# Optimization experiments

Hardware: AMD Instinct MI355X
Metric: run time of the kernel (lower is better)

Reference implementation:

```python
import jax, jax.numpy as jnp
import numpy as np

B, L, H = 8, 1024, 512
CHUNK = 16  # query-row chunk size for the score computation; L % CHUNK == 0


def setup_inputs() -> dict:
    key = jax.random.key(0)
    ks = jax.random.split(key, 6)
    s = 1.0 / np.sqrt(H)  # torch nn.Linear default init bound
    return {
        "inputs": jax.random.normal(ks[0], (B, L, H), jnp.float32),
        "W1": jax.random.uniform(ks[1], (H, H), jnp.float32, -s, s),
        "b1": jax.random.uniform(ks[2], (H,), jnp.float32, -s, s),
        "W2": jax.random.uniform(ks[3], (H, H), jnp.float32, -s, s),
        "b2": jax.random.uniform(ks[4], (H,), jnp.float32, -s, s),
        # torch: nn.init.normal_(q, mean=-0.02, std=0.02)
        "q": jax.random.normal(ks[5], (H,), jnp.float32) * 0.02 - 0.02,
    }


def _scores(u1, u2, q):
    # u[b,i,j] = tanh(u1[b,i,:] + u2[b,j,:]) . q  -- computed in row-chunks to
    # avoid materializing the full [B,L,L,H] tensor the torch loop implies.
    Bx, Lx, Hx = u1.shape
    n = Lx // CHUNK
    u1c = u1.reshape(Bx, n, CHUNK, Hx).transpose(1, 0, 2, 3)  # [n, B, c, H]

    def step(carry, u1_i):
        t = jnp.tanh(u1_i[:, :, None, :] + u2[:, None, :, :])  # [B, c, L, H]
        return carry, jnp.einsum('bclh,h->bcl', t, q)

    _, s = jax.lax.scan(jax.checkpoint(step), None, u1c)  # [n, B, c, L]
    return s.transpose(1, 0, 2, 3).reshape(Bx, Lx, Lx)


def reference(inputs, W1, b1, W2, b2, q):
    u1 = inputs @ W1.T + b1  # [B, L, H]
    u2 = inputs @ W2.T + b2  # [B, L, H]
    u = _scores(u1, u2, q)   # [B, L, L]
    # relu=False in init, so no relu on u
    a = jax.nn.softmax(u, axis=2)
    h = jnp.einsum('bij,bjh->bih', a, inputs)  # [B, L, H]
    return h, a
```

## Files before the change

kernel.cpp:

```cpp
#include <hip/hip_runtime.h>

typedef _Float16 f16;
typedef _Float16 f16x2 __attribute__((ext_vector_type(2)));
typedef _Float16 f16x4 __attribute__((ext_vector_type(4)));
typedef _Float16 f16x8 __attribute__((ext_vector_type(8)));
typedef float f32x4 __attribute__((ext_vector_type(4)));

#define LOG2E_X2 2.8853900817779268f

__constant__ float D8[8] = {0.543915f, 0.177997f, 0.0652351f, 0.0242575f,
                            0.00903807f, 0.00336823f, 0.00125536f, 0.000467884f};

static __device__ __forceinline__ void gl2lds16(const void* g, void* l) {
  __builtin_amdgcn_global_load_lds((const __attribute__((address_space(1))) void*)g,
                                   (__attribute__((address_space(3))) void*)l, 16, 0, 0);
}


__global__ __launch_bounds__(256) void k_prep_x(const float* __restrict__ X,
                                                f16* __restrict__ Xh, f16* __restrict__ XhT) {
  const int ht = blockIdx.x, it = blockIdx.y, b = blockIdx.z;
  __shared__ f16 Lt[64][72];
  const int t = threadIdx.x;
  const int r = t >> 4, c4 = (t & 15) * 4;
  const float* Xb = X + ((size_t)b * 1024 + it * 64) * 512 + ht * 64;
#pragma unroll
  for (int k = 0; k < 4; ++k) {
    const int rr = r + 16 * k;
    float4 v = *(const float4*)&Xb[(size_t)rr * 512 + c4];
    f16 h0 = (f16)v.x, h1 = (f16)v.y, h2 = (f16)v.z, h3 = (f16)v.w;
    *(f16x4*)&Xh[((size_t)b * 1024 + it * 64 + rr) * 512 + ht * 64 + c4] = {h0, h1, h2, h3};
    Lt[c4 + 0][rr] = h0; Lt[c4 + 1][rr] = h1; Lt[c4 + 2][rr] = h2; Lt[c4 + 3][rr] = h3;
  }
  __syncthreads();
  const int hr = t >> 2, seg = t & 3;
  f16* dst = &XhT[((size_t)b * 512 + ht * 64 + hr) * 1024 + it * 64 + seg * 16];
  *(f16x8*)(dst) = *(const f16x8*)&Lt[hr][seg * 16];
  *(f16x8*)(dst + 8) = *(const f16x8*)&Lt[hr][seg * 16 + 8];
}

__global__ __launch_bounds__(256) void k_prep_w(const float* __restrict__ W1,
                                                const float* __restrict__ W2,
                                                f16* __restrict__ Wh) {
  const int row = blockIdx.x, z = blockIdx.y, t = threadIdx.x;
  const float* W = z ? W2 : W1;
  float2 v = *(const float2*)&W[(size_t)row * 512 + t * 2];
  *(f16x2*)&Wh[(size_t)z * 262144 + (size_t)row * 512 + t * 2] = {(f16)v.x, (f16)v.y};
}

__global__ void k_prep_b(const float* __restrict__ b1, const float* __restrict__ b2,
                         float* __restrict__ biasCat) {
  const int t = blockIdx.x * 256 + threadIdx.x;
  biasCat[t] = t < 512 ? b1[t] : b2[t - 512];
}

template <int NM>
__global__ __launch_bounds__(256) void k_trig(const float* __restrict__ u,
                                              const float* __restrict__ q,
                                              f16* __restrict__ At, f16* __restrict__ Bt,
                                              float* __restrict__ qa, float* __restrict__ qb,
                                              int m0, int wq) {
  const int i = blockIdx.x, t = threadIdx.x;
  const float w = 0.62831853f;
  const float2 a2 = *(const float2*)&u[(size_t)i * 1024 + 2 * t];
  const float2 b2 = *(const float2*)&u[(size_t)i * 1024 + 512 + 2 * t];
  const float2 q2 = *(const float2*)&q[2 * t];
  if (wq) {
    float sa = q2.x * a2.x + q2.y * a2.y;
    float sb = q2.x * b2.x + q2.y * b2.y;
#pragma unroll
    for (int o = 1; o < 64; o <<= 1) { sa += __shfl_xor(sa, o); sb += __shfl_xor(sb, o); }
    __shared__ float red[8];
    const int lane = t & 63, widx = t >> 6;
    if (lane == 0) { red[widx] = sa; red[4 + widx] = sb; }
    __syncthreads();
    if (t == 0) qa[i] = red[0] + red[1] + red[2] + red[3];
    if (t == 1) qb[i] = red[4] + red[5] + red[6] + red[7];
  }
  float s1[4], c1[4], sm_[4], cm_[4];
  const float ang[4] = {w * a2.x, w * a2.y, w * b2.x, w * b2.y};
#pragma unroll
  for (int uu = 0; uu < 4; ++uu) {
    __sincosf(ang[uu], &s1[uu], &c1[uu]);
    if (m0 == 1) { sm_[uu] = s1[uu]; cm_[uu] = c1[uu]; }
    else __sincosf(m0 * ang[uu], &sm_[uu], &cm_[uu]);
  }
  const size_t ldT = (size_t)NM * 1024;
  f16* Ar = At + (size_t)i * ldT + 2 * t;
  f16* Br = Bt + (size_t)i * ldT + 2 * t;
#pragma unroll
  for (int j = 0; j < NM; ++j) {
    const float dm = D8[m0 - 1 + j];
    const float qdx = q2.x * dm, qdy = q2.y * dm;
    *(f16x2*)(Ar + j * 1024)       = {(f16)(qdx * sm_[0]), (f16)(qdy * sm_[1])};
    *(f16x2*)(Ar + j * 1024 + 512) = {(f16)(qdx * cm_[0]), (f16)(qdy * cm_[1])};
    *(f16x2*)(Br + j * 1024)       = {(f16)cm_[2], (f16)cm_[3]};
    *(f16x2*)(Br + j * 1024 + 512) = {(f16)sm_[2], (f16)sm_[3]};
    if (j + 1 < NM) {
#pragma unroll
      for (int uu = 0; uu < 4; ++uu) {
        const float ns = sm_[uu] * c1[uu] + cm_[uu] * s1[uu];
        const float nc = cm_[uu] * c1[uu] - sm_[uu] * s1[uu];
        sm_[uu] = ns; cm_[uu] = nc;
      }
    }
  }
}

template <int MODE, int ACC, int T, int WR, int WC, int FI, int FJ>
__global__ __launch_bounds__(T, 2) void k_gemmG(
    const f16* __restrict__ A, const f16* __restrict__ B, float* __restrict__ C,
    const float* __restrict__ bias0, int Kloop, int ldAB, long halfA, long halfC) {
  constexpr int BM = WR * FI * 16;
  constexpr int BN = WC * FJ * 16;
  __shared__ alignas(16) char smA[2][BM * 128];
  __shared__ alignas(16) char smB[2][BN * 128];
  const int t = threadIdx.x;
  int nx, my, z;
  if (MODE == 1) {
    const int lin = blockIdx.x;
    const int xcd = lin & 7, s = lin >> 3;
    const int g = xcd + 8 * (s >> 2);
    nx = s & 3; my = g & 3; z = g >> 2;
  } else {
    nx = blockIdx.x; my = blockIdx.y; z = blockIdx.z;
  }
  const f16* Ab; const f16* Bb; float* Cb; const float* bias = nullptr;
  int ldC;
  if (MODE == 0) {
    Ab = A + (size_t)my * BM * ldAB;
    Bb = B + (size_t)nx * BN * ldAB;
    Cb = C + (size_t)my * BM * 1024 + nx * BN;
    bias = bias0 + nx * BN;
    ldC = 1024;
  } else if (MODE == 1) {
    const int b = z & 7, h = z >> 3;
    Ab = A + ((size_t)(b * 1024 + my * 256)) * ldAB + h * halfA;
    Bb = B + ((size_t)(b * 1024 + nx * 256)) * ldAB + h * halfA;
    Cb = C + h * halfC + ((size_t)(b * 1024 + my * 256)) * 1024 + nx * 256;
    ldC = 1024;
  } else {
    Ab = A + (size_t)z * 1048576 + (size_t)my * BM * ldAB;
    Bb = B + (size_t)z * 524288 + (size_t)nx * BN * ldAB;
    Cb = C + (size_t)z * 524288 + (size_t)my * BM * 512 + nx * BN;
    ldC = 512;
  }
  const int wid = t >> 6, lane = t & 63;
  const int wr = wid / WC, wc = wid % WC;
  const int rl = lane & 15, kc = lane >> 4;
  f32x4 acc[FI][FJ] = {};

  auto stage = [&](int buf, int kt) {
    const f16* gA = Ab + kt * 64;
    const f16* gB = Bb + kt * 64;
    constexpr int LA = BM * 8 / T, LB = BN * 8 / T;
#pragma unroll
    for (int ii = 0; ii < LA; ++ii) {
      const int idx = ii * T + t;
      const int row = idx >> 3, c = idx & 7;
      gl2lds16(gA + (size_t)row * ldAB + ((c ^ (row & 7)) * 8),
               smA[buf] + ii * (T * 16) + wid * 1024);
    }
#pragma unroll
    for (int ii = 0; ii < LB; ++ii) {
      const int idx = ii * T + t;
      const int row = idx >> 3, c = idx & 7;
      gl2lds16(gB + (size_t)row * ldAB + ((c ^ (row & 7)) * 8),
               smB[buf] + ii * (T * 16) + wid * 1024);
    }
  };

  const int nkt = Kloop >> 6;
  stage(0, 0);
  __syncthreads();
  for (int kt = 0; kt < nkt; ++kt) {
    const int cur = kt & 1;
    if (kt + 1 < nkt) stage(cur ^ 1, kt + 1);
    const char* lA = smA[cur];
    const char* lB = smB[cur];
#pragma unroll
    for (int kk = 0; kk < 2; ++kk) {
      f16x8 av[FI], bv[FJ];
#pragma unroll
      for (int fi = 0; fi < FI; ++fi) {
        const int rloc = (wr * FI + fi) * 16 + rl;
        av[fi] = *(const f16x8*)(lA + rloc * 128 + (((kc + 4 * kk) ^ (rloc & 7)) << 4));
      }
#pragma unroll
      for (int fj = 0; fj < FJ; ++fj) {
        const int cloc = (wc * FJ + fj) * 16 + rl;
        bv[fj] = *(const f16x8*)(lB + cloc * 128 + (((kc + 4 * kk) ^ (cloc & 7)) << 4));
      }
#pragma unroll
      for (int fi = 0; fi < FI; ++fi)
#pragma unroll
        for (int fj = 0; fj < FJ; ++fj)
          acc[fi][fj] = __builtin_amdgcn_mfma_f32_16x16x32_f16(av[fi], bv[fj], acc[fi][fj], 0, 0, 0);
    }
    __syncthreads();
  }

#pragma unroll
  for (int fj = 0; fj < FJ; ++fj) {
    const int gcol = (wc * FJ + fj) * 16 + rl;
    const float bvv = (MODE == 0) ? bias[gcol] : 0.f;
#pragma unroll
    for (int fi = 0; fi < FI; ++fi) {
      const int grow0 = (wr * FI + fi) * 16 + kc * 4;
      f32x4 v = acc[fi][fj];
#pragma unroll
      for (int r = 0; r < 4; ++r) {
        const size_t o = (size_t)(grow0 + r) * ldC + gcol;
        float x = v[r] + bvv;
        if (ACC) x += Cb[o];
        Cb[o] = x;
      }
    }
  }
}

__global__ __launch_bounds__(256) void k_softmax2(const float* __restrict__ P0,
                                                  const float* __restrict__ P1,
                                                  const float* __restrict__ qa,
                                                  const float* __restrict__ qb,
                                                  float* __restrict__ out_a,
                                                  f16* __restrict__ a16) {
  const int row = blockIdx.x, t = threadIdx.x;
  const int b = row >> 10;
  const size_t off = (size_t)row * 1024 + t * 4;
  float4 p0 = *(const float4*)(P0 + off);
  float4 p1 = *(const float4*)(P1 + off);
  float4 qb4 = *(const float4*)(qb + (size_t)b * 1024 + t * 4);
  const float qi = qa[row];
  float4 v;
  v.x = p0.x + p1.x + 0.2f * (qi + qb4.x);
  v.y = p0.y + p1.y + 0.2f * (qi + qb4.y);
  v.z = p0.z + p1.z + 0.2f * (qi + qb4.z);
  v.w = p0.w + p1.w + 0.2f * (qi + qb4.w);
  float m = fmaxf(fmaxf(v.x, v.y), fmaxf(v.z, v.w));
#pragma unroll
  for (int o = 1; o < 64; o <<= 1) m = fmaxf(m, __shfl_xor(m, o));
  __shared__ float red[4];
  const int w = t >> 6, ln = t & 63;
  if (ln == 0) red[w] = m;
  __syncthreads();
  m = fmaxf(fmaxf(red[0], red[1]), fmaxf(red[2], red[3]));
  v.x = __expf(v.x - m); v.y = __expf(v.y - m);
  v.z = __expf(v.z - m); v.w = __expf(v.w - m);
  float s = v.x + v.y + v.z + v.w;
#pragma unroll
  for (int o = 1; o < 64; o <<= 1) s += __shfl_xor(s, o);
  __syncthreads();
  if (ln == 0) red[w] = s;
  __syncthreads();
  s = red[0] + red[1] + red[2] + red[3];
  const float inv = 1.0f / s;
  v.x *= inv; v.y *= inv; v.z *= inv; v.w *= inv;
  *(float4*)(out_a + off) = v;
  *(f16x4*)(a16 + off) = {(f16)v.x, (f16)v.y, (f16)v.z, (f16)v.w};
}

typedef short s16x2 __attribute__((ext_vector_type(2)));

static __device__ __forceinline__ float fdot2f(f16x2 a, f16x2 b, float c) {
#if __has_builtin(__builtin_amdgcn_fdot2)
  return __builtin_amdgcn_fdot2(a, b, c, false);
#else
  return c + (float)a[0] * (float)b[0] + (float)a[1] * (float)b[1];
#endif
}

__global__ void k_qprep(const float* __restrict__ q, f16* __restrict__ qh,
                        float* __restrict__ qsum) {
  const int t = threadIdx.x;
  float v = q[t];
  qh[t] = (f16)v;
  float s = v;
#pragma unroll
  for (int o = 1; o < 64; o <<= 1) s += __shfl_xor(s, o);
  __shared__ float red[8];
  if ((t & 63) == 0) red[t >> 6] = s;
  __syncthreads();
  if (t == 0) {
    float tot = 0.f;
#pragma unroll
    for (int i = 0; i < 8; ++i) tot += red[i];
    *qsum = tot;
  }
}

__global__ __launch_bounds__(256) void k_gemm_exp(
    const float* __restrict__ X, const float* __restrict__ W1,
    const float* __restrict__ b1, const float* __restrict__ W2,
    const float* __restrict__ b2, f16* __restrict__ e1, f16* __restrict__ e2) {
  const int z = blockIdx.z;
  const float* W = z ? W2 : W1;
  const float* bias = z ? b2 : b1;
  f16* out = z ? e2 : e1;
  const int r0 = blockIdx.y * 64;
  const int c0 = blockIdx.x * 64;
  __shared__ alignas(16) float Xs[64][68];
  __shared__ alignas(16) float Ws[64][68];
  const int t = threadIdx.x;
  const int row = t >> 2, seg = t & 3;
  const int tr = t >> 4, tc = t & 15;
  float acc[4][4] = {};
#pragma unroll 1
  for (int k0 = 0; k0 < 512; k0 += 64) {
    const float4* gx = (const float4*)(X + (size_t)(r0 + row) * 512 + k0 + seg * 16);
    float4* lx = (float4*)(&Xs[row][seg * 16]);
    lx[0] = gx[0]; lx[1] = gx[1]; lx[2] = gx[2]; lx[3] = gx[3];
    const float4* gw = (const float4*)(W + (size_t)(c0 + row) * 512 + k0 + seg * 16);
    float4* lw = (float4*)(&Ws[row][seg * 16]);
    lw[0] = gw[0]; lw[1] = gw[1]; lw[2] = gw[2]; lw[3] = gw[3];
    __syncthreads();
#pragma unroll 4
    for (int kk = 0; kk < 64; kk += 4) {
      float4 av[4], bv[4];
#pragma unroll
      for (int ii = 0; ii < 4; ++ii) av[ii] = *(const float4*)&Xs[tr + 16 * ii][kk];
#pragma unroll
      for (int jj = 0; jj < 4; ++jj) bv[jj] = *(const float4*)&Ws[tc + 16 * jj][kk];
#pragma unroll
      for (int ii = 0; ii < 4; ++ii) {
#pragma unroll
        for (int jj = 0; jj < 4; ++jj) {
          acc[ii][jj] = fmaf(av[ii].x, bv[jj].x, acc[ii][jj]);
          acc[ii][jj] = fmaf(av[ii].y, bv[jj].y, acc[ii][jj]);
          acc[ii][jj] = fmaf(av[ii].z, bv[jj].z, acc[ii][jj]);
          acc[ii][jj] = fmaf(av[ii].w, bv[jj].w, acc[ii][jj]);
        }
      }
    }
    __syncthreads();
  }
#pragma unroll
  for (int ii = 0; ii < 4; ++ii) {
    const int r = r0 + tr + 16 * ii;
#pragma unroll
    for (int jj = 0; jj < 4; ++jj) {
      const int c = c0 + tc + 16 * jj;
      float u = acc[ii][jj] + bias[c];
      float val = u * LOG2E_X2 - 4.0f;
      val = fminf(6.6759f, fmaxf(-14.6759f, val));
      out[(size_t)r * 512 + c] = (f16)exp2f(val);
    }
  }
}

template <int P>
static __device__ __forceinline__ void tanh_dot_step(const f16x8 (&Av)[4],
                                                     const f16x8 (&Bv)[4],
                                                     const f16x8& Qv, float (&acc)[4][4],
                                                     int c256, int kmag, int two2) {
  f16x2 qp = __builtin_shufflevector(Qv, Qv, 2 * P, 2 * P + 1);
#pragma unroll
  for (int jj = 0; jj < 4; ++jj) {
    f16x2 bp = __builtin_shufflevector(Bv[jj], Bv[jj], 2 * P, 2 * P + 1);
#pragma unroll
    for (int ii = 0; ii < 4; ++ii) {
      f16x2 ap = __builtin_shufflevector(Av[ii], Av[ii], 2 * P, 2 * P + 1);
      f16x2 d, r, tt;
      asm("v_pk_fma_f16 %0, %3, %4, %5\n\t"
          "v_pk_sub_i16 %1, %6, %0\n\t"
          "v_pk_fma_f16 %2, %0, %1, %7 neg_lo:[1,0,0] neg_hi:[1,0,0]\n\t"
          "v_pk_mul_f16 %1, %1, %2\n\t"
          "v_pk_fma_f16 %2, %0, %1, %7 neg_lo:[1,0,0] neg_hi:[1,0,0]\n\t"
          "v_pk_mul_f16 %1, %1, %2"
          : "=&v"(d), "=&v"(r), "=&v"(tt)
          : "v"(ap), "v"(bp), "v"(c256), "v"(kmag), "v"(two2));
      acc[ii][jj] = fdot2f(r, qp, acc[ii][jj]);
    }
  }
}

__global__ __launch_bounds__(256) void k_scores(const f16* __restrict__ e1,
                                                const f16* __restrict__ e2,
                                                const f16* __restrict__ qh,
                                                const float* __restrict__ qsum_p,
                                                float* __restrict__ out_a) {
  const int b = blockIdx.z, it = blockIdx.y, jt = blockIdx.x;
  __shared__ alignas(16) f16 As[64][72];
  __shared__ alignas(16) f16 Bs[64][72];
  __shared__ alignas(16) f16 Qs[512];
  const int t = threadIdx.x;
  const size_t eA = (size_t)(b * 1024 + it * 64) * 512;
  const size_t eB = (size_t)(b * 1024 + jt * 64) * 512;
  if (t < 64) ((uint4*)Qs)[t] = ((const uint4*)qh)[t];
  const int row = t >> 2, seg = t & 3;
  const int tr = t >> 4, tc = t & 15;
  const int c256 = 0x1C001C00;
  const int kmag = 0x77987798;
  const int two2 = 0x40004000;
  float acc[4][4] = {};
#pragma unroll 1
  for (int h0 = 0; h0 < 512; h0 += 64) {
    const f16* gA = e1 + eA + (size_t)row * 512 + h0;
    const f16* gB = e2 + eB + (size_t)row * 512 + h0;
    *(uint4*)(&As[row][seg * 8]) = *(const uint4*)(gA + seg * 8);
    *(uint4*)(&As[row][seg * 8 + 32]) = *(const uint4*)(gA + seg * 8 + 32);
    *(uint4*)(&Bs[row][seg * 8]) = *(const uint4*)(gB + seg * 8);
    *(uint4*)(&Bs[row][seg * 8 + 32]) = *(const uint4*)(gB + seg * 8 + 32);
    __syncthreads();
#pragma unroll 2
    for (int g = 0; g < 8; ++g) {
      f16x8 Av[4], Bv[4], Qv;
#pragma unroll
      for (int ii = 0; ii < 4; ++ii) Av[ii] = *(const f16x8*)&As[tr + 16 * ii][g * 8];
#pragma unroll
      for (int jj = 0; jj < 4; ++jj) Bv[jj] = *(const f16x8*)&Bs[tc + 16 * jj][g * 8];
      Qv = *(const f16x8*)&Qs[h0 + g * 8];
      tanh_dot_step<0>(Av, Bv, Qv, acc, c256, kmag, two2);
      tanh_dot_step<1>(Av, Bv, Qv, acc, c256, kmag, two2);
      tanh_dot_step<2>(Av, Bv, Qv, acc, c256, kmag, two2);
      tanh_dot_step<3>(Av, Bv, Qv, acc, c256, kmag, two2);
    }
    __syncthreads();
  }
  const float qs = *qsum_p;
#pragma unroll
  for (int ii = 0; ii < 4; ++ii) {
    const size_t orow = (size_t)(b * 1024 + it * 64 + tr + 16 * ii) * 1024;
#pragma unroll
    for (int jj = 0; jj < 4; ++jj)
      out_a[orow + jt * 64 + tc + 16 * jj] = qs - acc[ii][jj] * (1.0f / 128.0f);
  }
}

__global__ __launch_bounds__(256) void k_softmax(float* __restrict__ a) {
  float* row = a + (size_t)blockIdx.x * 1024;
  const int t = threadIdx.x;
  float4 v = ((const float4*)row)[t];
  float m = fmaxf(fmaxf(v.x, v.y), fmaxf(v.z, v.w));
#pragma unroll
  for (int o = 1; o < 64; o <<= 1) m = fmaxf(m, __shfl_xor(m, o));
  __shared__ float red[4];
  const int w = t >> 6, ln = t & 63;
  if (ln == 0) red[w] = m;
  __syncthreads();
  m = fmaxf(fmaxf(red[0], red[1]), fmaxf(red[2], red[3]));
  v.x = __expf(v.x - m); v.y = __expf(v.y - m);
  v.z = __expf(v.z - m); v.w = __expf(v.w - m);
  float s = v.x + v.y + v.z + v.w;
#pragma unroll
  for (int o = 1; o < 64; o <<= 1) s += __shfl_xor(s, o);
  __syncthreads();
  if (ln == 0) red[w] = s;
  __syncthreads();
  s = red[0] + red[1] + red[2] + red[3];
  const float inv = 1.0f / s;
  v.x *= inv; v.y *= inv; v.z *= inv; v.w *= inv;
  ((float4*)row)[t] = v;
}

__global__ __launch_bounds__(256) void k_av(const float* __restrict__ a,
                                            const float* __restrict__ X,
                                            float* __restrict__ h) {
  const int b = blockIdx.z;
  const int i0 = blockIdx.y * 64;
  const int c0 = blockIdx.x * 64;
  __shared__ alignas(16) float As[64][68];
  __shared__ alignas(16) float Xs[64][68];
  const float* Ab = a + (size_t)b * 1024 * 1024;
  const float* Xb = X + (size_t)b * 1024 * 512;
  const int t = threadIdx.x;
  const int row = t >> 2, seg = t & 3;
  const int tr = t >> 4, tc = t & 15;
  float acc[4][4] = {};
#pragma unroll 1
  for (int k0 = 0; k0 < 1024; k0 += 64) {
    const float4* ga = (const float4*)(Ab + (size_t)(i0 + row) * 1024 + k0 + seg * 16);
    float4* la = (float4*)(&As[row][seg * 16]);
    la[0] = ga[0]; la[1] = ga[1]; la[2] = ga[2]; la[3] = ga[3];
    const float4* gx = (const float4*)(Xb + (size_t)(k0 + row) * 512 + c0 + seg * 16);
    float4* lx = (float4*)(&Xs[row][seg * 16]);
    lx[0] = gx[0]; lx[1] = gx[1]; lx[2] = gx[2]; lx[3] = gx[3];
    __syncthreads();
#pragma unroll 8
    for (int k = 0; k < 64; ++k) {
      float av[4], bv[4];
#pragma unroll
      for (int ii = 0; ii < 4; ++ii) av[ii] = As[tr + 16 * ii][k];
#pragma unroll
      for (int jj = 0; jj < 4; ++jj) bv[jj] = Xs[k][tc + 16 * jj];
#pragma unroll
      for (int ii = 0; ii < 4; ++ii) {
#pragma unroll
        for (int jj = 0; jj < 4; ++jj)
          acc[ii][jj] = fmaf(av[ii], bv[jj], acc[ii][jj]);
      }
    }
    __syncthreads();
  }
#pragma unroll
  for (int ii = 0; ii < 4; ++ii) {
    const size_t orow = (size_t)b * 1024 * 512 + (size_t)(i0 + tr + 16 * ii) * 512;
#pragma unroll
    for (int jj = 0; jj < 4; ++jj)
      h[orow + c0 + tc + 16 * jj] = acc[ii][jj];
  }
}

extern "C" void kernel_launch(void* const* d_in, const int* in_sizes, int n_in,
                              void* d_out, int out_size, void* d_ws, size_t ws_size,
                              hipStream_t stream) {
  const float* inputs = (const float*)d_in[0];
  const float* W1 = (const float*)d_in[1];
  const float* b1 = (const float*)d_in[2];
  const float* W2 = (const float*)d_in[3];
  const float* b2 = (const float*)d_in[4];
  const float* q = (const float*)d_in[5];

  float* out_h = (float*)d_out;
  float* out_a = out_h + 4194304;

  const size_t FIXED = 101781504ULL;
  const size_t PER_M = 33554432ULL;
  if (ws_size < FIXED + PER_M) {
    char* ws = (char*)d_ws;
    f16* e1 = (f16*)ws;
    f16* e2 = (f16*)(ws + 8388608);
    f16* qh = (f16*)(ws + 16777216);
    float* qsum = (float*)(ws + 16778240);
    k_qprep<<<1, 512, 0, stream>>>(q, qh, qsum);
    k_gemm_exp<<<dim3(8, 128, 2), 256, 0, stream>>>(inputs, W1, b1, W2, b2, e1, e2);
    k_scores<<<dim3(16, 16, 8), 256, 0, stream>>>(e1, e2, qh, qsum, out_a);
    k_softmax<<<8192, 256, 0, stream>>>(out_a);
    k_av<<<dim3(8, 16, 8), 256, 0, stream>>>(out_a, inputs, out_h);
    return;
  }

  int nm = 8;
  while (FIXED + (size_t)nm * PER_M > ws_size) nm >>= 1;

  char* p = (char*)d_ws;
  f16* Xh = (f16*)p;            p += 8388608;
  f16* XhT = (f16*)p;           p += 8388608;
  f16* Wh = (f16*)p;            p += 1048576;
  f16* a16 = (f16*)p;           p += 16777216;
  float* qa = (float*)p;        p += 32768;
  float* qb = (float*)p;        p += 32768;
  float* biasCat = (float*)p;   p += 4096;
  float* P0 = (float*)p;        p += 33554432;
  float* P1 = (float*)p;        p += 33554432;
  f16* At = (f16*)p;            p += (size_t)nm * 16777216;
  f16* Bt = (f16*)p;

  float* u = out_a;

  k_prep_x<<<dim3(8, 16, 8), 256, 0, stream>>>(inputs, Xh, XhT);
  k_prep_w<<<dim3(512, 2), 256, 0, stream>>>(W1, W2, Wh);
  k_prep_b<<<4, 256, 0, stream>>>(b1, b2, biasCat);
  k_gemmG<0, 0, 512, 2, 4, 4, 4><<<dim3(4, 64, 1), 512, 0, stream>>>(
      Xh, Wh, u, biasCat, 512, 512, 0, 0);

  const int chunks = 8 / nm;
  for (int cch = 0; cch < chunks; ++cch) {
    const int m0 = cch * nm + 1;
    switch (nm) {
      case 8: k_trig<8><<<8192, 256, 0, stream>>>(u, q, At, Bt, qa, qb, m0, cch == 0); break;
      case 4: k_trig<4><<<8192, 256, 0, stream>>>(u, q, At, Bt, qa, qb, m0, cch == 0); break;
      case 2: k_trig<2><<<8192, 256, 0, stream>>>(u, q, At, Bt, qa, qb, m0, cch == 0); break;
      default: k_trig<1><<<8192, 256, 0, stream>>>(u, q, At, Bt, qa, qb, m0, cch == 0); break;
    }
    const int Kloop = nm * 512;
    const int ldAB = nm * 1024;
    const long halfA = (long)nm * 512;
    if (cch == 0)
      k_gemmG<1, 0, 512, 2, 4, 8, 4><<<dim3(256, 1, 1), 512, 0, stream>>>(
          At, Bt, P0, nullptr, Kloop, ldAB, halfA, 8388608L);
    else
      k_gemmG<1, 1, 512, 2, 4, 8, 4><<<dim3(256, 1, 1), 512, 0, stream>>>(
          At, Bt, P0, nullptr, Kloop, ldAB, halfA, 8388608L);
  }

  k_softmax2<<<8192, 256, 0, stream>>>(P0, P1, qa, qb, out_a, a16);
  k_gemmG<2, 0, 256, 2, 2, 4, 4><<<dim3(4, 8, 8), 256, 0, stream>>>(
      a16, XhT, out_h, nullptr, 1024, 1024, 0, 0);
}
```

Before: 295.7 us.

## Drop split-K in score GEMM and retile to 128x128 blocks

Result: slower. 313.2 us (+5.9%).

```diff
diff --git a/kernel.cpp b/kernel.cpp
--- a/kernel.cpp
+++ b/kernel.cpp
@@ -110,21 +110,13 @@
 template <int MODE, int ACC, int T, int WR, int WC, int FI, int FJ>
 __global__ __launch_bounds__(T, 2) void k_gemmG(
     const f16* __restrict__ A, const f16* __restrict__ B, float* __restrict__ C,
-    const float* __restrict__ bias0, int Kloop, int ldAB, long halfA, long halfC) {
+    const float* __restrict__ bias0, int Kloop, int ldAB) {
   constexpr int BM = WR * FI * 16;
   constexpr int BN = WC * FJ * 16;
   __shared__ alignas(16) char smA[2][BM * 128];
   __shared__ alignas(16) char smB[2][BN * 128];
   const int t = threadIdx.x;
-  int nx, my, z;
-  if (MODE == 1) {
-    const int lin = blockIdx.x;
-    const int xcd = lin & 7, s = lin >> 3;
-    const int g = xcd + 8 * (s >> 2);
-    nx = s & 3; my = g & 3; z = g >> 2;
-  } else {
-    nx = blockIdx.x; my = blockIdx.y; z = blockIdx.z;
-  }
+  const int nx = blockIdx.x, my = blockIdx.y, z = blockIdx.z;
   const f16* Ab; const f16* Bb; float* Cb; const float* bias = nullptr;
   int ldC;
   if (MODE == 0) {
@@ -134,10 +126,9 @@
     bias = bias0 + nx * BN;
     ldC = 1024;
   } else if (MODE == 1) {
-    const int b = z & 7, h = z >> 3;
-    Ab = A + ((size_t)(b * 1024 + my * 256)) * ldAB + h * halfA;
-    Bb = B + ((size_t)(b * 1024 + nx * 256)) * ldAB + h * halfA;
-    Cb = C + h * halfC + ((size_t)(b * 1024 + my * 256)) * 1024 + nx * 256;
+    Ab = A + ((size_t)(z * 1024 + my * BM)) * ldAB;
+    Bb = B + ((size_t)(z * 1024 + nx * BN)) * ldAB;
+    Cb = C + (size_t)z * 1048576 + (size_t)my * BM * 1024 + nx * BN;
     ldC = 1024;
   } else {
     Ab = A + (size_t)z * 1048576 + (size_t)my * BM * ldAB;
@@ -219,8 +210,7 @@
   }
 }
 
-__global__ __launch_bounds__(256) void k_softmax2(const float* __restrict__ P0,
-                                                  const float* __restrict__ P1,
+__global__ __launch_bounds__(256) void k_softmax2(const float* __restrict__ P,
                                                   const float* __restrict__ qa,
                                                   const float* __restrict__ qb,
                                                   float* __restrict__ out_a,
@@ -228,15 +218,14 @@
   const int row = blockIdx.x, t = threadIdx.x;
   const int b = row >> 10;
   const size_t off = (size_t)row * 1024 + t * 4;
-  float4 p0 = *(const float4*)(P0 + off);
-  float4 p1 = *(const float4*)(P1 + off);
+  float4 p0 = *(const float4*)(P + off);
   float4 qb4 = *(const float4*)(qb + (size_t)b * 1024 + t * 4);
   const float qi = qa[row];
   float4 v;
-  v.x = p0.x + p1.x + 0.2f * (qi + qb4.x);
-  v.y = p0.y + p1.y + 0.2f * (qi + qb4.y);
-  v.z = p0.z + p1.z + 0.2f * (qi + qb4.z);
-  v.w = p0.w + p1.w + 0.2f * (qi + qb4.w);
+  v.x = p0.x + 0.2f * (qi + qb4.x);
+  v.y = p0.y + 0.2f * (qi + qb4.y);
+  v.z = p0.z + 0.2f * (qi + qb4.z);
+  v.w = p0.w + 0.2f * (qi + qb4.w);
   float m = fmaxf(fmaxf(v.x, v.y), fmaxf(v.z, v.w));
 #pragma unroll
   for (int o = 1; o < 64; o <<= 1) m = fmaxf(m, __shfl_xor(m, o));
@@ -514,7 +503,7 @@
   float* out_h = (float*)d_out;
   float* out_a = out_h + 4194304;
 
-  const size_t FIXED = 101781504ULL;
+  const size_t FIXED = 68227072ULL;
   const size_t PER_M = 33554432ULL;
   if (ws_size < FIXED + PER_M) {
     char* ws = (char*)d_ws;
@@ -541,8 +530,7 @@
   float* qa = (float*)p;        p += 32768;
   float* qb = (float*)p;        p += 32768;
   float* biasCat = (float*)p;   p += 4096;
-  float* P0 = (float*)p;        p += 33554432;
-  float* P1 = (float*)p;        p += 33554432;
+  float* P = (float*)p;         p += 33554432;
   f16* At = (f16*)p;            p += (size_t)nm * 16777216;
   f16* Bt = (f16*)p;
 
@@ -552,7 +540,7 @@
   k_prep_w<<<dim3(512, 2), 256, 0, stream>>>(W1, W2, Wh);
   k_prep_b<<<4, 256, 0, stream>>>(b1, b2, biasCat);
   k_gemmG<0, 0, 512, 2, 4, 4, 4><<<dim3(4, 64, 1), 512, 0, stream>>>(
-      Xh, Wh, u, biasCat, 512, 512, 0, 0);
+      Xh, Wh, u, biasCat, 512, 512);
 
   const int chunks = 8 / nm;
   for (int cch = 0; cch < chunks; ++cch) {
@@ -563,18 +551,17 @@
       case 2: k_trig<2><<<8192, 256, 0, stream>>>(u, q, At, Bt, qa, qb, m0, cch == 0); break;
       default: k_trig<1><<<8192, 256, 0, stream>>>(u, q, At, Bt, qa, qb, m0, cch == 0); break;
     }
-    const int Kloop = nm * 512;
+    const int Kloop = nm * 1024;
     const int ldAB = nm * 1024;
-    const long halfA = (long)nm * 512;
     if (cch == 0)
-      k_gemmG<1, 0, 512, 2, 4, 8, 4><<<dim3(256, 1, 1), 512, 0, stream>>>(
-          At, Bt, P0, nullptr, Kloop, ldAB, halfA, 8388608L);
+      k_gemmG<1, 0, 256, 2, 2, 4, 4><<<dim3(8, 8, 8), 256, 0, stream>>>(
+          At, Bt, P, nullptr, Kloop, ldAB);
     else
-      k_gemmG<1, 1, 512, 2, 4, 8, 4><<<dim3(256, 1, 1), 512, 0, stream>>>(
-          At, Bt, P0, nullptr, Kloop, ldAB, halfA, 8388608L);
-  }
-
-  k_softmax2<<<8192, 256, 0, stream>>>(P0, P1, qa, qb, out_a, a16);
+      k_gemmG<1, 1, 256, 2, 2, 4, 4><<<dim3(8, 8, 8), 256, 0, stream>>>(
+          At, Bt, P, nullptr, Kloop, ldAB);
+  }
+
+  k_softmax2<<<8192, 256, 0, stream>>>(P, qa, qb, out_a, a16);
   k_gemmG<2, 0, 256, 2, 2, 4, 4><<<dim3(4, 8, 8), 256, 0, stream>>>(
-      a16, XhT, out_h, nullptr, 1024, 1024, 0, 0);
-}
+      a16, XhT, out_h, nullptr, 1024, 1024);
+}
```
